# Kernel tuning notes

Measured on AMD Instinct MI355X. Metric: run time of the kernel, lower is better.

The kernel has to match this reference:

```python
import jax, jax.numpy as jnp
import numpy as np

B, C_IN, C_OUT, H, W = 16, 256, 256, 64, 64
RANK, ORDER = 16, 2
EPS = 1e-5


def setup_inputs() -> dict:
    key = jax.random.key(0)
    k1, k2, k3 = jax.random.split(key, 3)
    x = jax.random.normal(k1, (B, C_IN, H, W), dtype=jnp.float32)
    # torch init: w_core ~ N(0, 1/(C_in*rank)), w_out ~ N(0, 1/rank)
    w_core = jax.random.normal(k2, (RANK, C_IN, RANK), dtype=jnp.float32) * (1.0 / (C_IN * RANK))
    w_out = jax.random.normal(k3, (RANK, C_OUT, RANK), dtype=jnp.float32) * (1.0 / RANK)
    return {"x": x, "w_core": w_core, "w_out": w_out}


def reference(x, w_core, w_out):
    # Per-pixel tensor-ring 1x1 conv.
    # Original chain for order=2 (share_core):
    #   T = einsum('achw,rck->arhwk', x, w_core)
    #   out = einsum('aebcf,afbcg,gdh->aedbch', T, T, w_out)
    #   y   = einsum('arohwr->aohw', out)   # ring trace over e==h
    # Equivalent: M[a,h,w] is rank x rank; P = M^order; y_d = tr(P @ W_d)
    M = jnp.einsum('achw,rck->ahwrk', x, w_core)  # [B,H,W,r,r]
    P = M
    for _ in range(ORDER - 1):
        P = jnp.einsum('ahwef,ahwfg->ahweg', P, M)
    y = jnp.einsum('ahweg,gde->adhw', P, w_out)  # [B,C_out,H,W]
    # InstanceNorm2d (affine=False, biased variance) + Softsign
    mean = jnp.mean(y, axis=(2, 3), keepdims=True)
    var = jnp.var(y, axis=(2, 3), keepdims=True)
    yn = (y - mean) * jax.lax.rsqrt(var + EPS)
    return yn / (1.0 + jnp.abs(yn))
```

## Files before the change

kernel.cpp:

```cpp
#include <hip/hip_runtime.h>

#define HW 4096
#define NC 256
#define ND 256
#define NB 16

typedef _Float16 half2_t __attribute__((ext_vector_type(2)));
typedef _Float16 half4_t __attribute__((ext_vector_type(4)));
typedef _Float16 half8_t __attribute__((ext_vector_type(8)));
typedef __fp16   fp16x2  __attribute__((ext_vector_type(2)));
typedef float floatx2 __attribute__((ext_vector_type(2)));
typedef float floatx4 __attribute__((ext_vector_type(4)));

#define MSCALE 64.0f
#define INV_MSCALE2 (1.0f / 4096.0f)
#define EPS_SCALED (1e-5f * 4096.0f * 4096.0f)

__global__ __launch_bounds__(256) void prep_weights(
        const float* __restrict__ w_core, const float* __restrict__ w_out,
        _Float16* __restrict__ W1p, _Float16* __restrict__ W2p,
        float* __restrict__ ssum) {
    int tid = blockIdx.x * 256 + threadIdx.x;
    if (tid < 8192) ssum[tid] = 0.f;
    int l   = tid & 63;
    int rt  = (tid >> 6) & 15;
    int ks  = (tid >> 10) & 7;
    int sel = tid >> 13;
    int row = l & 15, kg = l >> 4;
    half8_t v;
    if (sel == 0) {
        int r = rt, k = row;
#pragma unroll
        for (int j = 0; j < 8; ++j) {
            int c = ks * 32 + kg * 8 + j;
            v[j] = (_Float16)(w_core[r * 4096 + c * 16 + k] * MSCALE);
        }
        *(half8_t*)&W1p[(size_t)((ks * 16 + rt) * 64 + l) * 8] = v;
    } else {
        int d = rt * 16 + row;
#pragma unroll
        for (int j = 0; j < 8; ++j) {
            int eg = ks * 32 + kg * 8 + j, e = eg >> 4, g = eg & 15;
            v[j] = (_Float16)w_out[g * 4096 + d * 16 + e];
        }
        *(half8_t*)&W2p[(size_t)((ks * 16 + rt) * 64 + l) * 8] = v;
    }
}

template<bool F16Y>
__global__ __launch_bounds__(256, 2) void compute_y(
        const float* __restrict__ x, const _Float16* __restrict__ W1p,
        const _Float16* __restrict__ W2p, float* __restrict__ y,
        _Float16* __restrict__ y16, float* __restrict__ ssum,
        float* __restrict__ ssq) {
    __shared__ __align__(16) _Float16 S[16384];

    const int t = threadIdx.x;
    const int l = t & 63, w = t >> 6;
    const int a = blockIdx.x >> 6;
    const int pixbase = (blockIdx.x & 63) * 64;
    const int row16 = l & 15, kg = l >> 4;
    const float* xa = x + (size_t)a * NC * HW + pixbase;

    const half8_t* W1v = (const half8_t*)W1p;
    half8_t af[4], afn[4];
#pragma unroll
    for (int rq = 0; rq < 4; ++rq) af[rq] = W1v[(w * 4 + rq) * 64 + l];

    {
        const int px = t & 63;
        const int o0 = t >> 6;
#pragma unroll
        for (int h = 0; h < 2; ++h) {
            float xr[32];
#pragma unroll
            for (int q = 0; q < 4; ++q) {
                const int oct = (h * 4 + q) * 4 + o0;
#pragma unroll
                for (int j = 0; j < 8; ++j)
                    xr[q * 8 + j] = xa[(size_t)(oct * 8 + j) * HW + px];
            }
#pragma unroll
            for (int q = 0; q < 4; ++q) {
                const int oct = (h * 4 + q) * 4 + o0;
                half8_t hv;
#pragma unroll
                for (int j = 0; j < 8; ++j) hv[j] = (_Float16)xr[q * 8 + j];
                *(half8_t*)&S[px * 256 + ((oct ^ (px & 15)) << 3)] = hv;
            }
        }
    }
    __syncthreads();

    floatx4 acc[4][4];
#pragma unroll
    for (int i = 0; i < 4; ++i)
#pragma unroll
        for (int j = 0; j < 4; ++j) acc[i][j] = (floatx4){0.f, 0.f, 0.f, 0.f};
    for (int ks = 0; ks < 8; ++ks) {
        if (ks < 7) {
#pragma unroll
            for (int rq = 0; rq < 4; ++rq)
                afn[rq] = W1v[((ks + 1) * 16 + w * 4 + rq) * 64 + l];
        }
#pragma unroll
        for (int pt = 0; pt < 4; ++pt) {
            const int px = pt * 16 + row16;
            half8_t bf = *(const half8_t*)
                &S[px * 256 + (((ks * 4 + kg) ^ row16) << 3)];
#pragma unroll
            for (int rq = 0; rq < 4; ++rq)
                acc[rq][pt] = __builtin_amdgcn_mfma_f32_16x16x32_f16(
                                  af[rq], bf, acc[rq][pt], 0, 0, 0);
        }
#pragma unroll
        for (int rq = 0; rq < 4; ++rq) af[rq] = afn[rq];
    }

    const half8_t* W2v = (const half8_t*)W2p;
    half8_t caf[4], cafn[4];
#pragma unroll
    for (int dq = 0; dq < 4; ++dq) caf[dq] = W2v[(w * 4 + dq) * 64 + l];

    __syncthreads();

#pragma unroll
    for (int rq = 0; rq < 4; ++rq) {
        const int u = (w * 4 + rq) * 4 + kg;
#pragma unroll
        for (int pt = 0; pt < 4; ++pt) {
            const int px = pt * 16 + row16;
            half4_t hv;
#pragma unroll
            for (int r2 = 0; r2 < 4; ++r2) hv[r2] = (_Float16)acc[rq][pt][r2];
            *(half4_t*)&S[px * 256 + ((u ^ row16) << 2)] = hv;
        }
    }
    __syncthreads();

    {
        const int p = t >> 2, qe = t & 3, ps = p & 15;
        const _Float16* Mp = &S[p * 256];
        floatx2 Pacc[4][8];
#pragma unroll
        for (int i = 0; i < 4; ++i)
#pragma unroll
            for (int g2 = 0; g2 < 8; ++g2) Pacc[i][g2] = (floatx2){0.f, 0.f};
#pragma unroll
        for (int f4 = 0; f4 < 4; ++f4) {
            float Afb[4][4];
#pragma unroll
            for (int i = 0; i < 4; ++i) {
                const int e = i * 4 + qe;
                half4_t v = *(const half4_t*)
                    &Mp[(((e * 4 + f4) ^ ps) << 2)];
#pragma unroll
                for (int j = 0; j < 4; ++j) Afb[i][j] = (float)v[j];
            }
#pragma unroll
            for (int fl = 0; fl < 4; ++fl) {
                const int f = f4 * 4 + fl;
                floatx2 Bg[8];
#pragma unroll
                for (int g4 = 0; g4 < 4; ++g4) {
                    half4_t v = *(const half4_t*)
                        &Mp[(((f * 4 + g4) ^ ps) << 2)];
                    Bg[g4 * 2]     = (floatx2){(float)v[0], (float)v[1]};
                    Bg[g4 * 2 + 1] = (floatx2){(float)v[2], (float)v[3]};
                }
#pragma unroll
                for (int i = 0; i < 4; ++i) {
                    floatx2 a2 = {Afb[i][fl], Afb[i][fl]};
#pragma unroll
                    for (int g2 = 0; g2 < 8; ++g2)
                        Pacc[i][g2] = __builtin_elementwise_fma(a2, Bg[g2],
                                                                Pacc[i][g2]);
                }
            }
        }
#pragma unroll
        for (int i = 0; i < 4; ++i) {
            const int e = i * 4 + qe;
#pragma unroll
            for (int h2 = 0; h2 < 2; ++h2) {
                half8_t hv;
#pragma unroll
                for (int g2 = 0; g2 < 4; ++g2) {
                    fp16x2 pk = __builtin_amdgcn_cvt_pkrtz(
                        Pacc[i][h2 * 4 + g2][0], Pacc[i][h2 * 4 + g2][1]);
                    hv[g2 * 2]     = (_Float16)pk[0];
                    hv[g2 * 2 + 1] = (_Float16)pk[1];
                }
                *(half8_t*)&S[p * 256 + (((e * 2 + h2) ^ ps) << 3)] = hv;
            }
        }
    }
    __syncthreads();

    floatx4 cacc[4][4];
#pragma unroll
    for (int i = 0; i < 4; ++i)
#pragma unroll
        for (int j = 0; j < 4; ++j) cacc[i][j] = (floatx4){0.f, 0.f, 0.f, 0.f};
    for (int ks = 0; ks < 8; ++ks) {
        if (ks < 7) {
#pragma unroll
            for (int dq = 0; dq < 4; ++dq)
                cafn[dq] = W2v[((ks + 1) * 16 + w * 4 + dq) * 64 + l];
        }
#pragma unroll
        for (int pt = 0; pt < 4; ++pt) {
            const int px = pt * 16 + row16;
            half8_t bf = *(const half8_t*)
                &S[px * 256 + (((ks * 4 + kg) ^ row16) << 3)];
#pragma unroll
            for (int dq = 0; dq < 4; ++dq)
                cacc[dq][pt] = __builtin_amdgcn_mfma_f32_16x16x32_f16(
                                   caf[dq], bf, cacc[dq][pt], 0, 0, 0);
        }
#pragma unroll
        for (int dq = 0; dq < 4; ++dq) caf[dq] = cafn[dq];
    }

    float*     ya   = y   + (size_t)a * ND * HW + pixbase;
    _Float16*  ya16 = F16Y ? (y16 + (size_t)a * ND * HW + pixbase) : nullptr;
#pragma unroll
    for (int dq = 0; dq < 4; ++dq) {
        const int dbase = (w * 4 + dq) * 16 + kg * 4;
#pragma unroll
        for (int r2 = 0; r2 < 4; ++r2) {
            const int d = dbase + r2;
            float s = 0.f, q2 = 0.f;
#pragma unroll
            for (int pt = 0; pt < 4; ++pt) {
                float v;
                if (F16Y) {
                    _Float16 hv = (_Float16)cacc[dq][pt][r2];
                    ya16[(size_t)d * HW + pt * 16 + row16] = hv;
                    v = (float)hv;
                } else {
                    v = cacc[dq][pt][r2] * INV_MSCALE2;
                    ya[(size_t)d * HW + pt * 16 + row16] = v;
                }
                s += v; q2 += v * v;
            }
#pragma unroll
            for (int off = 1; off < 16; off <<= 1) {
                s  += __shfl_xor(s, off);
                q2 += __shfl_xor(q2, off);
            }
            if (row16 == 0) {
                atomicAdd(&ssum[a * 256 + d], s);
                atomicAdd(&ssq [a * 256 + d], q2);
            }
        }
    }
}

__global__ __launch_bounds__(256) void finalize_f16(
        const _Float16* __restrict__ y16, const float* __restrict__ ssum,
        const float* __restrict__ ssq, float* __restrict__ out) {
    const int ad = blockIdx.x;
    const float m  = ssum[ad] * (1.f / HW);
    const float sv = ssq[ad] * (1.f / HW) - m * m;
    const float s  = rsqrtf(sv + EPS_SCALED);
    const size_t base = (size_t)ad * HW + threadIdx.x * 16;
    half8_t h0 = *(const half8_t*)&y16[base];
    half8_t h1 = *(const half8_t*)&y16[base + 8];
    float o[16];
#pragma unroll
    for (int j = 0; j < 8; ++j) {
        float z0 = ((float)h0[j] - m) * s;
        float z1 = ((float)h1[j] - m) * s;
        o[j]     = z0 / (1.f + fabsf(z0));
        o[8 + j] = z1 / (1.f + fabsf(z1));
    }
#pragma unroll
    for (int q = 0; q < 4; ++q)
        *(float4*)&out[base + q * 4] =
            make_float4(o[q * 4], o[q * 4 + 1], o[q * 4 + 2], o[q * 4 + 3]);
}

__global__ __launch_bounds__(256) void finalize_f32(
        float* __restrict__ y, const float* __restrict__ ssum,
        const float* __restrict__ ssq) {
    const int i4 = blockIdx.x * 256 + threadIdx.x;
    const int ad = i4 >> 10;
    const float m  = ssum[ad] * (1.f / HW);
    const float sv = ssq[ad] * (1.f / HW) - m * m;
    const float s  = rsqrtf(sv + 1e-5f);
    float4 v = ((const float4*)y)[i4];
    float vv[4] = {v.x, v.y, v.z, v.w};
#pragma unroll
    for (int lq = 0; lq < 4; ++lq) {
        float z = (vv[lq] - m) * s;
        vv[lq] = z / (1.f + fabsf(z));
    }
    ((float4*)y)[i4] = make_float4(vv[0], vv[1], vv[2], vv[3]);
}

extern "C" void kernel_launch(void* const* d_in, const int* in_sizes, int n_in,
                              void* d_out, int out_size, void* d_ws, size_t ws_size,
                              hipStream_t stream) {
    const float* x      = (const float*)d_in[0];
    const float* w_core = (const float*)d_in[1];
    const float* w_out  = (const float*)d_in[2];
    float* y = (float*)d_out;

    char* wsb = (char*)d_ws;
    _Float16* W1p = (_Float16*)wsb;
    _Float16* W2p = (_Float16*)(wsb + 131072);
    float* ssum   = (float*)(wsb + 262144);
    float* ssq    = (float*)(wsb + 278528);
    _Float16* y16 = (_Float16*)(wsb + 294912);

    const size_t need_f16 = 294912 + (size_t)NB * ND * HW * sizeof(_Float16);
    const bool use_f16 = ws_size >= need_f16;

    prep_weights<<<64, 256, 0, stream>>>(w_core, w_out, W1p, W2p, ssum);
    if (use_f16) {
        compute_y<true><<<1024, 256, 0, stream>>>(x, W1p, W2p, y, y16, ssum, ssq);
        finalize_f16<<<4096, 256, 0, stream>>>(y16, ssum, ssq, y);
    } else {
        compute_y<false><<<1024, 256, 0, stream>>>(x, W1p, W2p, y, nullptr, ssum, ssq);
        finalize_f32<<<16384, 256, 0, stream>>>(y, ssum, ssq);
    }
}
```

Measured before the change: 81.26 us.

## Process two pixel tiles per block, prefetching next tile's x during compute

Each block now handles 128 pixels as two 64-pixel tiles, with shared memory doubled to hold a second buffer. While the first tile's matrix-square and output GEMM run, the second tile's x values are loaded from global memory into registers and written to the spare LDS buffer. The aim is to hide global load latency behind compute. The cost is half as many blocks, higher register pressure and 64KB of LDS per block, which may lower occupancy.

New measurement: 291.7 us. 3.59x slower.

```diff
diff --git a/kernel.cpp b/kernel.cpp
--- a/kernel.cpp
+++ b/kernel.cpp
@@ -53,207 +53,266 @@
         const _Float16* __restrict__ W2p, float* __restrict__ y,
         _Float16* __restrict__ y16, float* __restrict__ ssum,
         float* __restrict__ ssq) {
-    __shared__ __align__(16) _Float16 S[16384];
+    __shared__ __align__(16) _Float16 S[32768];
 
     const int t = threadIdx.x;
     const int l = t & 63, w = t >> 6;
-    const int a = blockIdx.x >> 6;
-    const int pixbase = (blockIdx.x & 63) * 64;
+    const int a  = blockIdx.x >> 5;
+    const int tp = blockIdx.x & 31;
+    const int pixbase0 = tp * 128;
     const int row16 = l & 15, kg = l >> 4;
-    const float* xa = x + (size_t)a * NC * HW + pixbase;
+    const float* xbase = x + (size_t)a * NC * HW;
 
     const half8_t* W1v = (const half8_t*)W1p;
-    half8_t af[4], afn[4];
+    const half8_t* W2v = (const half8_t*)W2p;
+
+    half8_t af[4], afn[4], caf[4], cafn[4];
 #pragma unroll
     for (int rq = 0; rq < 4; ++rq) af[rq] = W1v[(w * 4 + rq) * 64 + l];
 
+    const int sp = t & 63;
+    const int so = t >> 6;
+    const float* xa0 = xbase + pixbase0 + sp;
+    const float* xa1 = xbase + pixbase0 + 64 + sp;
+
     {
-        const int px = t & 63;
-        const int o0 = t >> 6;
 #pragma unroll
         for (int h = 0; h < 2; ++h) {
             float xr[32];
 #pragma unroll
             for (int q = 0; q < 4; ++q) {
-                const int oct = (h * 4 + q) * 4 + o0;
+                const int oct = (h * 4 + q) * 4 + so;
 #pragma unroll
                 for (int j = 0; j < 8; ++j)
-                    xr[q * 8 + j] = xa[(size_t)(oct * 8 + j) * HW + px];
+                    xr[q * 8 + j] = xa0[(size_t)(oct * 8 + j) * HW];
             }
 #pragma unroll
             for (int q = 0; q < 4; ++q) {
-                const int oct = (h * 4 + q) * 4 + o0;
+                const int oct = (h * 4 + q) * 4 + so;
                 half8_t hv;
 #pragma unroll
                 for (int j = 0; j < 8; ++j) hv[j] = (_Float16)xr[q * 8 + j];
-                *(half8_t*)&S[px * 256 + ((oct ^ (px & 15)) << 3)] = hv;
+                *(half8_t*)&S[sp * 256 + ((oct ^ (sp & 15)) << 3)] = hv;
             }
         }
     }
     __syncthreads();
 
-    floatx4 acc[4][4];
-#pragma unroll
-    for (int i = 0; i < 4; ++i)
-#pragma unroll
-        for (int j = 0; j < 4; ++j) acc[i][j] = (floatx4){0.f, 0.f, 0.f, 0.f};
-    for (int ks = 0; ks < 8; ++ks) {
-        if (ks < 7) {
-#pragma unroll
-            for (int rq = 0; rq < 4; ++rq)
-                afn[rq] = W1v[((ks + 1) * 16 + w * 4 + rq) * 64 + l];
-        }
-#pragma unroll
-        for (int pt = 0; pt < 4; ++pt) {
-            const int px = pt * 16 + row16;
-            half8_t bf = *(const half8_t*)
-                &S[px * 256 + (((ks * 4 + kg) ^ row16) << 3)];
-#pragma unroll
-            for (int rq = 0; rq < 4; ++rq)
-                acc[rq][pt] = __builtin_amdgcn_mfma_f32_16x16x32_f16(
-                                  af[rq], bf, acc[rq][pt], 0, 0, 0);
-        }
-#pragma unroll
-        for (int rq = 0; rq < 4; ++rq) af[rq] = afn[rq];
-    }
-
-    const half8_t* W2v = (const half8_t*)W2p;
-    half8_t caf[4], cafn[4];
-#pragma unroll
-    for (int dq = 0; dq < 4; ++dq) caf[dq] = W2v[(w * 4 + dq) * 64 + l];
-
-    __syncthreads();
-
-#pragma unroll
-    for (int rq = 0; rq < 4; ++rq) {
-        const int u = (w * 4 + rq) * 4 + kg;
-#pragma unroll
-        for (int pt = 0; pt < 4; ++pt) {
-            const int px = pt * 16 + row16;
-            half4_t hv;
-#pragma unroll
-            for (int r2 = 0; r2 < 4; ++r2) hv[r2] = (_Float16)acc[rq][pt][r2];
-            *(half4_t*)&S[px * 256 + ((u ^ row16) << 2)] = hv;
-        }
-    }
-    __syncthreads();
-
-    {
-        const int p = t >> 2, qe = t & 3, ps = p & 15;
-        const _Float16* Mp = &S[p * 256];
-        floatx2 Pacc[4][8];
+#pragma unroll 1
+    for (int tt = 0; tt < 2; ++tt) {
+        _Float16* R  = S + tt * 16384;
+        _Float16* Rn = S + 16384;
+        const int pixbase = pixbase0 + tt * 64;
+
+        floatx4 acc[4][4];
 #pragma unroll
         for (int i = 0; i < 4; ++i)
 #pragma unroll
-            for (int g2 = 0; g2 < 8; ++g2) Pacc[i][g2] = (floatx2){0.f, 0.f};
-#pragma unroll
-        for (int f4 = 0; f4 < 4; ++f4) {
-            float Afb[4][4];
+            for (int j = 0; j < 4; ++j) acc[i][j] = (floatx4){0.f, 0.f, 0.f, 0.f};
+        for (int ks = 0; ks < 8; ++ks) {
+            if (ks < 7) {
+#pragma unroll
+                for (int rq = 0; rq < 4; ++rq)
+                    afn[rq] = W1v[((ks + 1) * 16 + w * 4 + rq) * 64 + l];
+            }
+#pragma unroll
+            for (int pt = 0; pt < 4; ++pt) {
+                const int px = pt * 16 + row16;
+                half8_t bf = *(const half8_t*)
+                    &R[px * 256 + (((ks * 4 + kg) ^ row16) << 3)];
+#pragma unroll
+                for (int rq = 0; rq < 4; ++rq)
+                    acc[rq][pt] = __builtin_amdgcn_mfma_f32_16x16x32_f16(
+                                      af[rq], bf, acc[rq][pt], 0, 0, 0);
+            }
+#pragma unroll
+            for (int rq = 0; rq < 4; ++rq) af[rq] = afn[rq];
+        }
+
+#pragma unroll
+        for (int dq = 0; dq < 4; ++dq) caf[dq] = W2v[(w * 4 + dq) * 64 + l];
+
+        __syncthreads();
+
+#pragma unroll
+        for (int rq = 0; rq < 4; ++rq) {
+            const int u = (w * 4 + rq) * 4 + kg;
+#pragma unroll
+            for (int pt = 0; pt < 4; ++pt) {
+                const int px = pt * 16 + row16;
+                half4_t hv;
+#pragma unroll
+                for (int r2 = 0; r2 < 4; ++r2) hv[r2] = (_Float16)acc[rq][pt][r2];
+                *(half4_t*)&S[(tt * 16384) + px * 256 + ((u ^ row16) << 2)] = hv;
+            }
+        }
+        __syncthreads();
+
+        float xr1[32];
+        {
+            const int p = t >> 2, qe = t & 3, ps = p & 15;
+            const _Float16* Mp = &R[p * 256];
+
+            float xr0[32];
+            if (tt == 0) {
+#pragma unroll
+                for (int q = 0; q < 4; ++q) {
+                    const int oct = 4 * q + so;
+#pragma unroll
+                    for (int j = 0; j < 8; ++j)
+                        xr0[q * 8 + j] = xa1[(size_t)(oct * 8 + j) * HW];
+                }
+            }
+
+            floatx2 Pacc[4][8];
+#pragma unroll
+            for (int i = 0; i < 4; ++i)
+#pragma unroll
+                for (int g2 = 0; g2 < 8; ++g2) Pacc[i][g2] = (floatx2){0.f, 0.f};
+#pragma unroll
+            for (int f4 = 0; f4 < 4; ++f4) {
+                float Afb[4][4];
+#pragma unroll
+                for (int i = 0; i < 4; ++i) {
+                    const int e = i * 4 + qe;
+                    half4_t v = *(const half4_t*)
+                        &Mp[(((e * 4 + f4) ^ ps) << 2)];
+#pragma unroll
+                    for (int j = 0; j < 4; ++j) Afb[i][j] = (float)v[j];
+                }
+#pragma unroll
+                for (int fl = 0; fl < 4; ++fl) {
+                    const int f = f4 * 4 + fl;
+                    floatx2 Bg[8];
+#pragma unroll
+                    for (int g4 = 0; g4 < 4; ++g4) {
+                        half4_t v = *(const half4_t*)
+                            &Mp[(((f * 4 + g4) ^ ps) << 2)];
+                        Bg[g4 * 2]     = (floatx2){(float)v[0], (float)v[1]};
+                        Bg[g4 * 2 + 1] = (floatx2){(float)v[2], (float)v[3]};
+                    }
+#pragma unroll
+                    for (int i = 0; i < 4; ++i) {
+                        floatx2 a2 = {Afb[i][fl], Afb[i][fl]};
+#pragma unroll
+                        for (int g2 = 0; g2 < 8; ++g2)
+                            Pacc[i][g2] = __builtin_elementwise_fma(a2, Bg[g2],
+                                                                    Pacc[i][g2]);
+                    }
+                }
+            }
+
+            if (tt == 0) {
+#pragma unroll
+                for (int q = 0; q < 4; ++q) {
+                    const int oct = 4 * q + so;
+                    half8_t hv;
+#pragma unroll
+                    for (int j = 0; j < 8; ++j) hv[j] = (_Float16)xr0[q * 8 + j];
+                    *(half8_t*)&Rn[sp * 256 + ((oct ^ (sp & 15)) << 3)] = hv;
+                }
+#pragma unroll
+                for (int q = 0; q < 4; ++q) {
+                    const int oct = 16 + 4 * q + so;
+#pragma unroll
+                    for (int j = 0; j < 8; ++j)
+                        xr1[q * 8 + j] = xa1[(size_t)(oct * 8 + j) * HW];
+                }
+            }
+
 #pragma unroll
             for (int i = 0; i < 4; ++i) {
                 const int e = i * 4 + qe;
-                half4_t v = *(const half4_t*)
-                    &Mp[(((e * 4 + f4) ^ ps) << 2)];
-#pragma unroll
-                for (int j = 0; j < 4; ++j) Afb[i][j] = (float)v[j];
-            }
-#pragma unroll
-            for (int fl = 0; fl < 4; ++fl) {
-                const int f = f4 * 4 + fl;
-                floatx2 Bg[8];
-#pragma unroll
-                for (int g4 = 0; g4 < 4; ++g4) {
-                    half4_t v = *(const half4_t*)
-                        &Mp[(((f * 4 + g4) ^ ps) << 2)];
-                    Bg[g4 * 2]     = (floatx2){(float)v[0], (float)v[1]};
-                    Bg[g4 * 2 + 1] = (floatx2){(float)v[2], (float)v[3]};
-                }
-#pragma unroll
-                for (int i = 0; i < 4; ++i) {
-                    floatx2 a2 = {Afb[i][fl], Afb[i][fl]};
-#pragma unroll
-                    for (int g2 = 0; g2 < 8; ++g2)
-                        Pacc[i][g2] = __builtin_elementwise_fma(a2, Bg[g2],
-                                                                Pacc[i][g2]);
-                }
-            }
-        }
-#pragma unroll
-        for (int i = 0; i < 4; ++i) {
-            const int e = i * 4 + qe;
-#pragma unroll
-            for (int h2 = 0; h2 < 2; ++h2) {
+#pragma unroll
+                for (int h2 = 0; h2 < 2; ++h2) {
+                    half8_t hv;
+#pragma unroll
+                    for (int g2 = 0; g2 < 4; ++g2) {
+                        fp16x2 pk = __builtin_amdgcn_cvt_pkrtz(
+                            Pacc[i][h2 * 4 + g2][0], Pacc[i][h2 * 4 + g2][1]);
+                        hv[g2 * 2]     = (_Float16)pk[0];
+                        hv[g2 * 2 + 1] = (_Float16)pk[1];
+                    }
+                    *(half8_t*)&R[p * 256 + (((e * 2 + h2) ^ ps) << 3)] = hv;
+                }
+            }
+        }
+        __syncthreads();
+
+        if (tt == 0) {
+#pragma unroll
+            for (int q = 0; q < 4; ++q) {
+                const int oct = 16 + 4 * q + so;
                 half8_t hv;
 #pragma unroll
-                for (int g2 = 0; g2 < 4; ++g2) {
-                    fp16x2 pk = __builtin_amdgcn_cvt_pkrtz(
-                        Pacc[i][h2 * 4 + g2][0], Pacc[i][h2 * 4 + g2][1]);
-                    hv[g2 * 2]     = (_Float16)pk[0];
-                    hv[g2 * 2 + 1] = (_Float16)pk[1];
-                }
-                *(half8_t*)&S[p * 256 + (((e * 2 + h2) ^ ps) << 3)] = hv;
-            }
-        }
-    }
-    __syncthreads();
-
-    floatx4 cacc[4][4];
-#pragma unroll
-    for (int i = 0; i < 4; ++i)
-#pragma unroll
-        for (int j = 0; j < 4; ++j) cacc[i][j] = (floatx4){0.f, 0.f, 0.f, 0.f};
-    for (int ks = 0; ks < 8; ++ks) {
-        if (ks < 7) {
-#pragma unroll
-            for (int dq = 0; dq < 4; ++dq)
-                cafn[dq] = W2v[((ks + 1) * 16 + w * 4 + dq) * 64 + l];
-        }
-#pragma unroll
-        for (int pt = 0; pt < 4; ++pt) {
-            const int px = pt * 16 + row16;
-            half8_t bf = *(const half8_t*)
-                &S[px * 256 + (((ks * 4 + kg) ^ row16) << 3)];
-#pragma unroll
-            for (int dq = 0; dq < 4; ++dq)
-                cacc[dq][pt] = __builtin_amdgcn_mfma_f32_16x16x32_f16(
-                                   caf[dq], bf, cacc[dq][pt], 0, 0, 0);
-        }
-#pragma unroll
-        for (int dq = 0; dq < 4; ++dq) caf[dq] = cafn[dq];
-    }
-
-    float*     ya   = y   + (size_t)a * ND * HW + pixbase;
-    _Float16*  ya16 = F16Y ? (y16 + (size_t)a * ND * HW + pixbase) : nullptr;
-#pragma unroll
-    for (int dq = 0; dq < 4; ++dq) {
-        const int dbase = (w * 4 + dq) * 16 + kg * 4;
-#pragma unroll
-        for (int r2 = 0; r2 < 4; ++r2) {
-            const int d = dbase + r2;
-            float s = 0.f, q2 = 0.f;
+                for (int j = 0; j < 8; ++j) hv[j] = (_Float16)xr1[q * 8 + j];
+                *(half8_t*)&Rn[sp * 256 + ((oct ^ (sp & 15)) << 3)] = hv;
+            }
+        }
+
+        floatx4 cacc[4][4];
+#pragma unroll
+        for (int i = 0; i < 4; ++i)
+#pragma unroll
+            for (int j = 0; j < 4; ++j) cacc[i][j] = (floatx4){0.f, 0.f, 0.f, 0.f};
+        for (int ks = 0; ks < 8; ++ks) {
+            if (ks < 7) {
+#pragma unroll
+                for (int dq = 0; dq < 4; ++dq)
+                    cafn[dq] = W2v[((ks + 1) * 16 + w * 4 + dq) * 64 + l];
+            }
 #pragma unroll
             for (int pt = 0; pt < 4; ++pt) {
-                float v;
-                if (F16Y) {
-                    _Float16 hv = (_Float16)cacc[dq][pt][r2];
-                    ya16[(size_t)d * HW + pt * 16 + row16] = hv;
-                    v = (float)hv;
-                } else {
-                    v = cacc[dq][pt][r2] * INV_MSCALE2;
-                    ya[(size_t)d * HW + pt * 16 + row16] = v;
-                }
-                s += v; q2 += v * v;
-            }
-#pragma unroll
-            for (int off = 1; off < 16; off <<= 1) {
-                s  += __shfl_xor(s, off);
-                q2 += __shfl_xor(q2, off);
-            }
-            if (row16 == 0) {
-                atomicAdd(&ssum[a * 256 + d], s);
-                atomicAdd(&ssq [a * 256 + d], q2);
-            }
-        }
+                const int px = pt * 16 + row16;
+                half8_t bf = *(const half8_t*)
+                    &R[px * 256 + (((ks * 4 + kg) ^ row16) << 3)];
+#pragma unroll
+                for (int dq = 0; dq < 4; ++dq)
+                    cacc[dq][pt] = __builtin_amdgcn_mfma_f32_16x16x32_f16(
+                                       caf[dq], bf, cacc[dq][pt], 0, 0, 0);
+            }
+#pragma unroll
+            for (int dq = 0; dq < 4; ++dq) caf[dq] = cafn[dq];
+        }
+
+        float*    ya   = y   + (size_t)a * ND * HW + pixbase;
+        _Float16* ya16 = F16Y ? (y16 + (size_t)a * ND * HW + pixbase) : nullptr;
+        if (tt == 0) {
+#pragma unroll
+            for (int rq = 0; rq < 4; ++rq) af[rq] = W1v[(w * 4 + rq) * 64 + l];
+        }
+#pragma unroll
+        for (int dq = 0; dq < 4; ++dq) {
+            const int dbase = (w * 4 + dq) * 16 + kg * 4;
+#pragma unroll
+            for (int r2 = 0; r2 < 4; ++r2) {
+                const int d = dbase + r2;
+                float s = 0.f, q2 = 0.f;
+#pragma unroll
+                for (int pt = 0; pt < 4; ++pt) {
+                    float v;
+                    if (F16Y) {
+                        _Float16 hv = (_Float16)cacc[dq][pt][r2];
+                        ya16[(size_t)d * HW + pt * 16 + row16] = hv;
+                        v = (float)hv;
+                    } else {
+                        v = cacc[dq][pt][r2] * INV_MSCALE2;
+                        ya[(size_t)d * HW + pt * 16 + row16] = v;
+                    }
+                    s += v; q2 += v * v;
+                }
+#pragma unroll
+                for (int off = 1; off < 16; off <<= 1) {
+                    s  += __shfl_xor(s, off);
+                    q2 += __shfl_xor(q2, off);
+                }
+                if (row16 == 0) {
+                    atomicAdd(&ssum[a * 256 + d], s);
+                    atomicAdd(&ssq [a * 256 + d], q2);
+                }
+            }
+        }
+        if (tt == 0) __syncthreads();
     }
 }
 
@@ -319,10 +378,10 @@
 
     prep_weights<<<64, 256, 0, stream>>>(w_core, w_out, W1p, W2p, ssum);
     if (use_f16) {
-        compute_y<true><<<1024, 256, 0, stream>>>(x, W1p, W2p, y, y16, ssum, ssq);
+        compute_y<true><<<512, 256, 0, stream>>>(x, W1p, W2p, y, y16, ssum, ssq);
         finalize_f16<<<4096, 256, 0, stream>>>(y16, ssum, ssq, y);
     } else {
-        compute_y<false><<<1024, 256, 0, stream>>>(x, W1p, W2p, y, nullptr, ssum, ssq);
+        compute_y<false><<<512, 256, 0, stream>>>(x, W1p, W2p, y, nullptr, ssum, ssq);
         finalize_f32<<<16384, 256, 0, stream>>>(y, ssum, ssq);
     }
 }
```
